# Performance work log

Measured on AMD Instinct MI355X. Metric: run time of the kernel, lower is better.

## Reference

```python
import jax, jax.numpy as jnp
import numpy as np

N_NODES = 100000
N_EDGES = 300000
F = 256


def setup_inputs() -> dict:
    key = jax.random.key(0)
    k1, k2, k3, k4, k5, k6 = jax.random.split(key, 6)
    x = jax.random.normal(k1, (N_NODES, F), dtype=jnp.float32)
    edge_index = jax.random.randint(k2, (2, N_EDGES), 0, N_NODES, dtype=jnp.int32)
    # GCNConv learned params (PyG: lin weight [out,in] applied as x @ W.T; store as [in,out])
    W_conv = jax.random.normal(k3, (F, F), dtype=jnp.float32) / np.sqrt(F)
    b_conv = jax.random.normal(k4, (F,), dtype=jnp.float32) * 0.01
    W_lin = jax.random.normal(k5, (F, 1), dtype=jnp.float32) / np.sqrt(F)
    b_lin = jax.random.normal(k6, (1,), dtype=jnp.float32) * 0.01
    return {"x": x, "edge_index": edge_index, "W_conv": W_conv,
            "b_conv": b_conv, "W_lin": W_lin, "b_lin": b_lin}


def gcn_conv(x, edge_index, W_conv, b_conv):
    N = x.shape[0]
    # add self loops (PyG default add_self_loops=True)
    loop = jnp.arange(N, dtype=edge_index.dtype)
    src = jnp.concatenate([edge_index[0], loop])
    dst = jnp.concatenate([edge_index[1], loop])
    # symmetric normalization: deg over destination, norm = d^-1/2[src]*d^-1/2[dst]
    deg = jax.ops.segment_sum(jnp.ones_like(dst, dtype=x.dtype), dst, num_segments=N)
    dinv = jnp.where(deg > 0, jax.lax.rsqrt(deg), 0.0)
    norm = dinv[src] * dinv[dst]  # [E+N]
    h = x @ W_conv  # [N,F] dense transform first (PyG order)
    msg = h[src] * norm[:, None]  # gather + scale, [E+N, F]
    agg = jax.ops.segment_sum(msg, dst, num_segments=N)  # scatter-add, [N,F]
    return agg + b_conv


def reference(x, edge_index, W_conv, b_conv, W_lin, b_lin):
    h = jax.nn.relu(gcn_conv(x, edge_index, W_conv, b_conv))
    return jax.nn.sigmoid(h @ W_lin + b_lin)  # [N,1]
```

## Files before the change

kernel.cpp:

```cpp
#include <hip/hip_runtime.h>
#include <hip/hip_bf16.h>
#include <math.h>

#define FDIM 256

typedef short bfrag __attribute__((ext_vector_type(8)));
typedef float f32x4 __attribute__((ext_vector_type(4)));

__device__ __forceinline__ short f2bf_rne(float f) {
    uint32_t u = __float_as_uint(f);
    uint32_t r = (u + 0x7FFFu + ((u >> 16) & 1u)) >> 16;
    return (short)r;
}
__device__ __forceinline__ float bf2f(short s) {
    return __uint_as_float(((uint32_t)(uint16_t)s) << 16);
}

#define GLOAD_LDS16(g, l) __builtin_amdgcn_global_load_lds(              \
    (const __attribute__((address_space(1))) void*)(g),                  \
    (__attribute__((address_space(3))) void*)(l), 16, 0, 0)

__global__ void count_kernel(const int* __restrict__ dst, int* __restrict__ counts, int E) {
    int e = blockIdx.x * 256 + threadIdx.x;
    if (e < E) atomicAdd(&counts[dst[e]], 1);
}

__global__ void scan1_kernel(const int* __restrict__ counts, int* __restrict__ blksums, int N) {
    __shared__ int sd[256];
    int tid = threadIdx.x;
    int base = blockIdx.x * 1024 + tid * 4;
    int s = 0;
#pragma unroll
    for (int t = 0; t < 4; ++t) { int i = base + t; if (i < N) s += counts[i]; }
    sd[tid] = s; __syncthreads();
    for (int off = 128; off > 0; off >>= 1) {
        if (tid < off) sd[tid] += sd[tid + off];
        __syncthreads();
    }
    if (tid == 0) blksums[blockIdx.x] = sd[0];
}

__global__ void scan2_kernel(int* __restrict__ blksums, int NB) {
    __shared__ int sd[128];
    int tid = threadIdx.x;
    int v = (tid < NB) ? blksums[tid] : 0;
    sd[tid] = v; __syncthreads();
    for (int off = 1; off < 128; off <<= 1) {
        int t = (tid >= off) ? sd[tid - off] : 0;
        __syncthreads();
        sd[tid] += t;
        __syncthreads();
    }
    if (tid < NB) blksums[tid] = sd[tid] - v;
}

__global__ void scan3_kernel(const int* __restrict__ counts, const int* __restrict__ blksums,
                             int* __restrict__ offsets, int* __restrict__ cursor,
                             float* __restrict__ dinv, int N, int E) {
    __shared__ int sd[256];
    int tid = threadIdx.x;
    int base = blockIdx.x * 1024 + tid * 4;
    int c[4]; int s = 0;
#pragma unroll
    for (int t = 0; t < 4; ++t) { int i = base + t; c[t] = (i < N) ? counts[i] : 0; s += c[t]; }
    sd[tid] = s; __syncthreads();
    int v = s;
    for (int off = 1; off < 256; off <<= 1) {
        int t = (tid >= off) ? sd[tid - off] : 0;
        __syncthreads();
        sd[tid] += t;
        __syncthreads();
    }
    int run = sd[tid] - v + blksums[blockIdx.x];
#pragma unroll
    for (int t = 0; t < 4; ++t) {
        int i = base + t;
        if (i < N) {
            offsets[i] = run;
            cursor[i]  = run;
            dinv[i] = rsqrtf((float)(c[t] + 1));
            run += c[t];
        }
    }
    if (blockIdx.x == 0 && tid == 0) offsets[N] = E;
}

__global__ void fill_kernel(const int* __restrict__ src, const int* __restrict__ dst,
                            int* __restrict__ cursor, const float* __restrict__ dinv,
                            int* __restrict__ csr_src, float* __restrict__ csr_norm, int E) {
    int e = blockIdx.x * 256 + threadIdx.x;
    if (e < E) {
        int s = src[e], d = dst[e];
        int pos = atomicAdd(&cursor[d], 1);
        csr_src[pos]  = s;
        csr_norm[pos] = dinv[s] * dinv[d];
    }
}

__global__ void wsplit_kernel(const float* __restrict__ W,
                              short* __restrict__ Wh, short* __restrict__ Wl) {
    const int k = blockIdx.x;
    const int n = threadIdx.x;
    const float w = W[k * 256 + n];
    const short hi = f2bf_rne(w);
    const short lo = f2bf_rne(w - bf2f(hi));
    const int s = k >> 5, g = (k & 31) >> 3, j = k & 7;
    const size_t idx = (size_t)s * 8192 + g * 2048 + n * 8 + j;
    Wh[idx] = hi; Wl[idx] = lo;
}

__global__ __launch_bounds__(512) void gemm_mfma(const float* __restrict__ X,
                                                 const short* __restrict__ Wth,
                                                 const short* __restrict__ Wtl,
                                                 float* __restrict__ H, int N) {
    __shared__ short Xh[4096], Xl[4096];
    __shared__ short Wh[8192], Wl[8192];

    const int tid  = threadIdx.x;
    const int lane = tid & 63;
    const int wid  = tid >> 6;
    const int wm   = wid >> 2;
    const int wn   = wid & 3;
    const int row0 = blockIdx.x * 128;

    const int sm = tid >> 2, sc = tid & 3;

    f32x4 acc[4][4];
#pragma unroll
    for (int i = 0; i < 4; ++i)
#pragma unroll
        for (int j = 0; j < 4; ++j) acc[i][j] = (f32x4){0.f, 0.f, 0.f, 0.f};

    float4 xv0, xv1;
    {
        const int row = row0 + sm;
        if (row < N) {
            const float* s = X + (size_t)row * FDIM + 8 * sc;
            xv0 = *(const float4*)s; xv1 = *(const float4*)(s + 4);
        } else { xv0 = make_float4(0,0,0,0); xv1 = make_float4(0,0,0,0); }
    }

    const int g   = lane >> 4;
    const int r15 = lane & 15;

    for (int s = 0; s < 8; ++s) {
        {
            const float v[8] = {xv0.x, xv0.y, xv0.z, xv0.w, xv1.x, xv1.y, xv1.z, xv1.w};
            bfrag hi8, lo8;
#pragma unroll
            for (int j = 0; j < 8; ++j) {
                const short h = f2bf_rne(v[j]);
                hi8[j] = h;
                lo8[j] = f2bf_rne(v[j] - bf2f(h));
            }
            *(bfrag*)(&Xh[(sc * 128 + sm) * 8]) = hi8;
            *(bfrag*)(&Xl[(sc * 128 + sm) * 8]) = lo8;
        }
        {
            const short* gh = Wth + s * 8192;
            const short* gl = Wtl + s * 8192;
            const int seg = wid * 512 + lane * 8;
#pragma unroll
            for (int p = 0; p < 2; ++p) {
                GLOAD_LDS16(gh + p * 4096 + seg, &Wh[p * 4096 + wid * 512]);
                GLOAD_LDS16(gl + p * 4096 + seg, &Wl[p * 4096 + wid * 512]);
            }
        }
        __syncthreads();

        if (s < 7) {
            const int row = row0 + sm;
            if (row < N) {
                const float* src = X + (size_t)row * FDIM + (s + 1) * 32 + 8 * sc;
                xv0 = *(const float4*)src; xv1 = *(const float4*)(src + 4);
            } else { xv0 = make_float4(0,0,0,0); xv1 = make_float4(0,0,0,0); }
        }

        bfrag bh[4], bl[4];
#pragma unroll
        for (int ni = 0; ni < 4; ++ni) {
            const int off = (g * 256 + wn * 64 + ni * 16 + r15) * 8;
            bh[ni] = *(const bfrag*)(&Wh[off]);
            bl[ni] = *(const bfrag*)(&Wl[off]);
        }
#pragma unroll
        for (int mi = 0; mi < 4; ++mi) {
            const int off = (g * 128 + wm * 64 + mi * 16 + r15) * 8;
            const bfrag ah = *(const bfrag*)(&Xh[off]);
            const bfrag al = *(const bfrag*)(&Xl[off]);
#pragma unroll
            for (int ni = 0; ni < 4; ++ni) {
                acc[mi][ni] = __builtin_amdgcn_mfma_f32_16x16x32_bf16(ah, bh[ni], acc[mi][ni], 0, 0, 0);
                acc[mi][ni] = __builtin_amdgcn_mfma_f32_16x16x32_bf16(ah, bl[ni], acc[mi][ni], 0, 0, 0);
                acc[mi][ni] = __builtin_amdgcn_mfma_f32_16x16x32_bf16(al, bh[ni], acc[mi][ni], 0, 0, 0);
            }
        }
        __syncthreads();
    }

#pragma unroll
    for (int mi = 0; mi < 4; ++mi) {
        const int rowb = row0 + wm * 64 + mi * 16 + g * 4;
#pragma unroll
        for (int r = 0; r < 4; ++r) {
            const int row = rowb + r;
            if (row < N) {
                float* base = H + (size_t)row * FDIM + wn * 64 + r15;
#pragma unroll
                for (int ni = 0; ni < 4; ++ni) base[ni * 16] = acc[mi][ni][r];
            }
        }
    }
}

__global__ __launch_bounds__(256) void agg_kernel(const float* __restrict__ h,
                                                  const int* __restrict__ offsets,
                                                  const int* __restrict__ csr_src,
                                                  const float* __restrict__ csr_norm,
                                                  const float* __restrict__ dinv,
                                                  const float* __restrict__ b_conv,
                                                  const float* __restrict__ W_lin,
                                                  const float* __restrict__ b_lin,
                                                  float* __restrict__ out, int N) {
    const int wid  = threadIdx.x >> 6;
    const int lane = threadIdx.x & 63;
    const int node = blockIdx.x * 4 + wid;
    if (node >= N) return;

    const float4* __restrict__ h4 = (const float4*)h;
    float4 acc = {0.f, 0.f, 0.f, 0.f};

    const int start = offsets[node];
    const int end   = offsets[node + 1];
    const float di  = dinv[node];

    for (int j = start; j < end; ++j) {
        const int s   = csr_src[j];
        const float w = csr_norm[j];
        const float4 v = h4[(size_t)s * 64 + lane];
        acc.x = fmaf(v.x, w, acc.x);
        acc.y = fmaf(v.y, w, acc.y);
        acc.z = fmaf(v.z, w, acc.z);
        acc.w = fmaf(v.w, w, acc.w);
    }
    {
        const float w = di * di;
        const float4 v = h4[(size_t)node * 64 + lane];
        acc.x = fmaf(v.x, w, acc.x);
        acc.y = fmaf(v.y, w, acc.y);
        acc.z = fmaf(v.z, w, acc.z);
        acc.w = fmaf(v.w, w, acc.w);
    }
    const float4 bc = ((const float4*)b_conv)[lane];
    acc.x = fmaxf(acc.x + bc.x, 0.f);
    acc.y = fmaxf(acc.y + bc.y, 0.f);
    acc.z = fmaxf(acc.z + bc.z, 0.f);
    acc.w = fmaxf(acc.w + bc.w, 0.f);

    const float4 wl = ((const float4*)W_lin)[lane];
    float p = acc.x * wl.x + acc.y * wl.y + acc.z * wl.z + acc.w * wl.w;
#pragma unroll
    for (int off = 32; off > 0; off >>= 1) p += __shfl_xor(p, off);
    if (lane == 0) out[node] = 1.f / (1.f + expf(-(p + b_lin[0])));
}

extern "C" void kernel_launch(void* const* d_in, const int* in_sizes, int n_in,
                              void* d_out, int out_size, void* d_ws, size_t ws_size,
                              hipStream_t stream) {
    const float* x      = (const float*)d_in[0];
    const int*   eidx   = (const int*)d_in[1];
    const float* W_conv = (const float*)d_in[2];
    const float* b_conv = (const float*)d_in[3];
    const float* W_lin  = (const float*)d_in[4];
    const float* b_lin  = (const float*)d_in[5];
    float* out = (float*)d_out;

    const int N = in_sizes[0] / FDIM;
    const int E = in_sizes[1] / 2;
    const int* e_src = eidx;
    const int* e_dst = eidx + E;

    char* p = (char*)d_ws;
    float* h = (float*)p;           p += (size_t)N * FDIM * sizeof(float);
    int* counts   = (int*)p;        p += (size_t)N * sizeof(int);
    int* offsets  = (int*)p;        p += (size_t)(N + 1) * sizeof(int);
    int* cursor   = (int*)p;        p += (size_t)N * sizeof(int);
    float* dinv   = (float*)p;      p += (size_t)N * sizeof(float);
    int* csr_src  = (int*)p;        p += (size_t)E * sizeof(int);
    float* csr_norm = (float*)p;    p += (size_t)E * sizeof(float);
    int* blksums  = (int*)p;        p += 128 * sizeof(int);
    short* Wth    = (short*)p;      p += (size_t)FDIM * FDIM * sizeof(short);
    short* Wtl    = (short*)p;      p += (size_t)FDIM * FDIM * sizeof(short);

    const int NB = (N + 1023) / 1024;

    hipMemsetAsync(counts, 0, (size_t)N * sizeof(int), stream);

    count_kernel<<<(E + 255) / 256, 256, 0, stream>>>(e_dst, counts, E);
    scan1_kernel<<<NB, 256, 0, stream>>>(counts, blksums, N);
    scan2_kernel<<<1, 128, 0, stream>>>(blksums, NB);
    scan3_kernel<<<NB, 256, 0, stream>>>(counts, blksums, offsets, cursor, dinv, N, E);
    fill_kernel<<<(E + 255) / 256, 256, 0, stream>>>(e_src, e_dst, cursor, dinv,
                                                     csr_src, csr_norm, E);

    wsplit_kernel<<<FDIM, FDIM, 0, stream>>>(W_conv, Wth, Wtl);

    gemm_mfma<<<(N + 127) / 128, 512, 0, stream>>>(x, Wth, Wtl, h, N);

    agg_kernel<<<(N + 3) / 4, 256, 0, stream>>>(h, offsets, csr_src, csr_norm, dinv,
                                                b_conv, W_lin, b_lin, out, N);
}
```

Before: 309.3 us.

## Store H as bf16, double-buffer GEMM LDS, change W/X layout, unroll aggregation

The GEMM now writes its output H in bf16 rather than fp32, which halves H's write traffic and the gather traffic in the aggregation kernel. The GEMM also double-buffers its X and W tiles in LDS, prefetching the next stage while the current one computes, and switches to a row-major k-interleaved fragment layout. The aggregation loop is unrolled by two with independent accumulators. Rounding H to bf16 adds error relative to the fp32 reference, and the doubled LDS footprint may reduce occupancy.

Result: faster. 286.8 us (-7.3%).

```diff
diff --git a/kernel.cpp b/kernel.cpp
--- a/kernel.cpp
+++ b/kernel.cpp
@@ -12,8 +12,8 @@
     uint32_t r = (u + 0x7FFFu + ((u >> 16) & 1u)) >> 16;
     return (short)r;
 }
-__device__ __forceinline__ float bf2f(short s) {
-    return __uint_as_float(((uint32_t)(uint16_t)s) << 16);
+__device__ __forceinline__ float bf2f(unsigned short s) {
+    return __uint_as_float(((uint32_t)s) << 16);
 }
 
 #define GLOAD_LDS16(g, l) __builtin_amdgcn_global_load_lds(              \
@@ -103,18 +103,18 @@
     const int n = threadIdx.x;
     const float w = W[k * 256 + n];
     const short hi = f2bf_rne(w);
-    const short lo = f2bf_rne(w - bf2f(hi));
+    const short lo = f2bf_rne(w - bf2f((unsigned short)hi));
     const int s = k >> 5, g = (k & 31) >> 3, j = k & 7;
-    const size_t idx = (size_t)s * 8192 + g * 2048 + n * 8 + j;
+    const size_t idx = (size_t)s * 8192 + n * 32 + g * 8 + j;
     Wh[idx] = hi; Wl[idx] = lo;
 }
 
 __global__ __launch_bounds__(512) void gemm_mfma(const float* __restrict__ X,
                                                  const short* __restrict__ Wth,
                                                  const short* __restrict__ Wtl,
-                                                 float* __restrict__ H, int N) {
-    __shared__ short Xh[4096], Xl[4096];
-    __shared__ short Wh[8192], Wl[8192];
+                                                 unsigned short* __restrict__ Hb, int N) {
+    __shared__ short Xh[2][4096], Xl[2][4096];
+    __shared__ short Wh[2][8192], Wl[2][8192];
 
     const int tid  = threadIdx.x;
     const int lane = tid & 63;
@@ -122,8 +122,9 @@
     const int wm   = wid >> 2;
     const int wn   = wid & 3;
     const int row0 = blockIdx.x * 128;
-
-    const int sm = tid >> 2, sc = tid & 3;
+    const int sm   = tid >> 2;
+    const int g    = lane >> 4;
+    const int r15  = lane & 15;
 
     f32x4 acc[4][4];
 #pragma unroll
@@ -131,63 +132,71 @@
 #pragma unroll
         for (int j = 0; j < 4; ++j) acc[i][j] = (f32x4){0.f, 0.f, 0.f, 0.f};
 
-    float4 xv0, xv1;
+    const int xrow = row0 + sm;
+    const float* xbase = X + (size_t)xrow * FDIM + 8 * (tid & 3);
+
+    float4 xa0, xa1;
+    if (xrow < N) { xa0 = *(const float4*)xbase; xa1 = *(const float4*)(xbase + 4); }
+    else          { xa0 = make_float4(0,0,0,0); xa1 = make_float4(0,0,0,0); }
     {
-        const int row = row0 + sm;
-        if (row < N) {
-            const float* s = X + (size_t)row * FDIM + 8 * sc;
-            xv0 = *(const float4*)s; xv1 = *(const float4*)(s + 4);
-        } else { xv0 = make_float4(0,0,0,0); xv1 = make_float4(0,0,0,0); }
-    }
-
-    const int g   = lane >> 4;
-    const int r15 = lane & 15;
+        const float v[8] = {xa0.x,xa0.y,xa0.z,xa0.w,xa1.x,xa1.y,xa1.z,xa1.w};
+        bfrag hi8, lo8;
+#pragma unroll
+        for (int j = 0; j < 8; ++j) {
+            const short h = f2bf_rne(v[j]);
+            hi8[j] = h; lo8[j] = f2bf_rne(v[j] - bf2f((unsigned short)h));
+        }
+        *(bfrag*)(&Xh[0][tid * 8]) = hi8;
+        *(bfrag*)(&Xl[0][tid * 8]) = lo8;
+    }
+#pragma unroll
+    for (int p = 0; p < 2; ++p) {
+        GLOAD_LDS16(Wth + p * 4096 + wid * 512 + lane * 8, &Wh[0][p * 4096 + wid * 512]);
+        GLOAD_LDS16(Wtl + p * 4096 + wid * 512 + lane * 8, &Wl[0][p * 4096 + wid * 512]);
+    }
+    if (xrow < N) { xa0 = *(const float4*)(xbase + 32); xa1 = *(const float4*)(xbase + 36); }
+    else          { xa0 = make_float4(0,0,0,0); xa1 = make_float4(0,0,0,0); }
+    __syncthreads();
 
     for (int s = 0; s < 8; ++s) {
-        {
-            const float v[8] = {xv0.x, xv0.y, xv0.z, xv0.w, xv1.x, xv1.y, xv1.z, xv1.w};
+        const int cur = s & 1, nxt = cur ^ 1;
+        if (s < 7) {
+            const float v[8] = {xa0.x,xa0.y,xa0.z,xa0.w,xa1.x,xa1.y,xa1.z,xa1.w};
             bfrag hi8, lo8;
 #pragma unroll
             for (int j = 0; j < 8; ++j) {
                 const short h = f2bf_rne(v[j]);
-                hi8[j] = h;
-                lo8[j] = f2bf_rne(v[j] - bf2f(h));
+                hi8[j] = h; lo8[j] = f2bf_rne(v[j] - bf2f((unsigned short)h));
             }
-            *(bfrag*)(&Xh[(sc * 128 + sm) * 8]) = hi8;
-            *(bfrag*)(&Xl[(sc * 128 + sm) * 8]) = lo8;
-        }
-        {
-            const short* gh = Wth + s * 8192;
-            const short* gl = Wtl + s * 8192;
-            const int seg = wid * 512 + lane * 8;
+            *(bfrag*)(&Xh[nxt][tid * 8]) = hi8;
+            *(bfrag*)(&Xl[nxt][tid * 8]) = lo8;
+            const short* gh = Wth + (s + 1) * 8192;
+            const short* gl = Wtl + (s + 1) * 8192;
 #pragma unroll
             for (int p = 0; p < 2; ++p) {
-                GLOAD_LDS16(gh + p * 4096 + seg, &Wh[p * 4096 + wid * 512]);
-                GLOAD_LDS16(gl + p * 4096 + seg, &Wl[p * 4096 + wid * 512]);
+                GLOAD_LDS16(gh + p * 4096 + wid * 512 + lane * 8, &Wh[nxt][p * 4096 + wid * 512]);
+                GLOAD_LDS16(gl + p * 4096 + wid * 512 + lane * 8, &Wl[nxt][p * 4096 + wid * 512]);
             }
         }
-        __syncthreads();
-
-        if (s < 7) {
-            const int row = row0 + sm;
-            if (row < N) {
-                const float* src = X + (size_t)row * FDIM + (s + 1) * 32 + 8 * sc;
-                xv0 = *(const float4*)src; xv1 = *(const float4*)(src + 4);
-            } else { xv0 = make_float4(0,0,0,0); xv1 = make_float4(0,0,0,0); }
+        if (s < 6) {
+            if (xrow < N) {
+                const float* src = xbase + (s + 2) * 32;
+                xa0 = *(const float4*)src; xa1 = *(const float4*)(src + 4);
+            } else { xa0 = make_float4(0,0,0,0); xa1 = make_float4(0,0,0,0); }
         }
 
         bfrag bh[4], bl[4];
 #pragma unroll
         for (int ni = 0; ni < 4; ++ni) {
-            const int off = (g * 256 + wn * 64 + ni * 16 + r15) * 8;
-            bh[ni] = *(const bfrag*)(&Wh[off]);
-            bl[ni] = *(const bfrag*)(&Wl[off]);
+            const int off = ((wn * 64 + ni * 16 + r15) * 4 + g) * 8;
+            bh[ni] = *(const bfrag*)(&Wh[cur][off]);
+            bl[ni] = *(const bfrag*)(&Wl[cur][off]);
         }
 #pragma unroll
         for (int mi = 0; mi < 4; ++mi) {
-            const int off = (g * 128 + wm * 64 + mi * 16 + r15) * 8;
-            const bfrag ah = *(const bfrag*)(&Xh[off]);
-            const bfrag al = *(const bfrag*)(&Xl[off]);
+            const int off = ((wm * 64 + mi * 16 + r15) * 4 + g) * 8;
+            const bfrag ah = *(const bfrag*)(&Xh[cur][off]);
+            const bfrag al = *(const bfrag*)(&Xl[cur][off]);
 #pragma unroll
             for (int ni = 0; ni < 4; ++ni) {
                 acc[mi][ni] = __builtin_amdgcn_mfma_f32_16x16x32_bf16(ah, bh[ni], acc[mi][ni], 0, 0, 0);
@@ -195,7 +204,7 @@
                 acc[mi][ni] = __builtin_amdgcn_mfma_f32_16x16x32_bf16(al, bh[ni], acc[mi][ni], 0, 0, 0);
             }
         }
-        __syncthreads();
+        if (s < 7) __syncthreads();
     }
 
 #pragma unroll
@@ -205,15 +214,16 @@
         for (int r = 0; r < 4; ++r) {
             const int row = rowb + r;
             if (row < N) {
-                float* base = H + (size_t)row * FDIM + wn * 64 + r15;
-#pragma unroll
-                for (int ni = 0; ni < 4; ++ni) base[ni * 16] = acc[mi][ni][r];
+                unsigned short* base = Hb + (size_t)row * FDIM + wn * 64 + r15;
+#pragma unroll
+                for (int ni = 0; ni < 4; ++ni)
+                    base[ni * 16] = (unsigned short)f2bf_rne(acc[mi][ni][r]);
             }
         }
     }
 }
 
-__global__ __launch_bounds__(256) void agg_kernel(const float* __restrict__ h,
+__global__ __launch_bounds__(256) void agg_kernel(const unsigned short* __restrict__ hb,
                                                   const int* __restrict__ offsets,
                                                   const int* __restrict__ csr_src,
                                                   const float* __restrict__ csr_norm,
@@ -227,38 +237,45 @@
     const int node = blockIdx.x * 4 + wid;
     if (node >= N) return;
 
-    const float4* __restrict__ h4 = (const float4*)h;
-    float4 acc = {0.f, 0.f, 0.f, 0.f};
+    float a0 = 0.f, a1 = 0.f, a2 = 0.f, a3 = 0.f;
+    float c0 = 0.f, c1 = 0.f, c2 = 0.f, c3 = 0.f;
 
     const int start = offsets[node];
     const int end   = offsets[node + 1];
     const float di  = dinv[node];
 
-    for (int j = start; j < end; ++j) {
-        const int s   = csr_src[j];
-        const float w = csr_norm[j];
-        const float4 v = h4[(size_t)s * 64 + lane];
-        acc.x = fmaf(v.x, w, acc.x);
-        acc.y = fmaf(v.y, w, acc.y);
-        acc.z = fmaf(v.z, w, acc.z);
-        acc.w = fmaf(v.w, w, acc.w);
+    int j = start;
+    for (; j + 1 < end; j += 2) {
+        const int   s0 = csr_src[j],     s1 = csr_src[j + 1];
+        const float w0 = csr_norm[j],    w1 = csr_norm[j + 1];
+        const ushort4 v0 = *((const ushort4*)(hb + (size_t)s0 * FDIM) + lane);
+        const ushort4 v1 = *((const ushort4*)(hb + (size_t)s1 * FDIM) + lane);
+        a0 = fmaf(bf2f(v0.x), w0, a0); a1 = fmaf(bf2f(v0.y), w0, a1);
+        a2 = fmaf(bf2f(v0.z), w0, a2); a3 = fmaf(bf2f(v0.w), w0, a3);
+        c0 = fmaf(bf2f(v1.x), w1, c0); c1 = fmaf(bf2f(v1.y), w1, c1);
+        c2 = fmaf(bf2f(v1.z), w1, c2); c3 = fmaf(bf2f(v1.w), w1, c3);
+    }
+    if (j < end) {
+        const int   s0 = csr_src[j];
+        const float w0 = csr_norm[j];
+        const ushort4 v0 = *((const ushort4*)(hb + (size_t)s0 * FDIM) + lane);
+        a0 = fmaf(bf2f(v0.x), w0, a0); a1 = fmaf(bf2f(v0.y), w0, a1);
+        a2 = fmaf(bf2f(v0.z), w0, a2); a3 = fmaf(bf2f(v0.w), w0, a3);
     }
     {
         const float w = di * di;
-        const float4 v = h4[(size_t)node * 64 + lane];
-        acc.x = fmaf(v.x, w, acc.x);
-        acc.y = fmaf(v.y, w, acc.y);
-        acc.z = fmaf(v.z, w, acc.z);
-        acc.w = fmaf(v.w, w, acc.w);
-    }
+        const ushort4 v = *((const ushort4*)(hb + (size_t)node * FDIM) + lane);
+        a0 = fmaf(bf2f(v.x), w, a0); a1 = fmaf(bf2f(v.y), w, a1);
+        a2 = fmaf(bf2f(v.z), w, a2); a3 = fmaf(bf2f(v.w), w, a3);
+    }
+    a0 += c0; a1 += c1; a2 += c2; a3 += c3;
+
     const float4 bc = ((const float4*)b_conv)[lane];
-    acc.x = fmaxf(acc.x + bc.x, 0.f);
-    acc.y = fmaxf(acc.y + bc.y, 0.f);
-    acc.z = fmaxf(acc.z + bc.z, 0.f);
-    acc.w = fmaxf(acc.w + bc.w, 0.f);
+    a0 = fmaxf(a0 + bc.x, 0.f); a1 = fmaxf(a1 + bc.y, 0.f);
+    a2 = fmaxf(a2 + bc.z, 0.f); a3 = fmaxf(a3 + bc.w, 0.f);
 
     const float4 wl = ((const float4*)W_lin)[lane];
-    float p = acc.x * wl.x + acc.y * wl.y + acc.z * wl.z + acc.w * wl.w;
+    float p = a0 * wl.x + a1 * wl.y + a2 * wl.z + a3 * wl.w;
 #pragma unroll
     for (int off = 32; off > 0; off >>= 1) p += __shfl_xor(p, off);
     if (lane == 0) out[node] = 1.f / (1.f + expf(-(p + b_lin[0])));
@@ -281,7 +298,7 @@
     const int* e_dst = eidx + E;
 
     char* p = (char*)d_ws;
-    float* h = (float*)p;           p += (size_t)N * FDIM * sizeof(float);
+    unsigned short* hb = (unsigned short*)p; p += (size_t)N * FDIM * sizeof(unsigned short);
     int* counts   = (int*)p;        p += (size_t)N * sizeof(int);
     int* offsets  = (int*)p;        p += (size_t)(N + 1) * sizeof(int);
     int* cursor   = (int*)p;        p += (size_t)N * sizeof(int);
@@ -305,8 +322,8 @@
 
     wsplit_kernel<<<FDIM, FDIM, 0, stream>>>(W_conv, Wth, Wtl);
 
-    gemm_mfma<<<(N + 127) / 128, 512, 0, stream>>>(x, Wth, Wtl, h, N);
-
-    agg_kernel<<<(N + 3) / 4, 256, 0, stream>>>(h, offsets, csr_src, csr_norm, dinv,
+    gemm_mfma<<<(N + 127) / 128, 512, 0, stream>>>(x, Wth, Wtl, hb, N);
+
+    agg_kernel<<<(N + 3) / 4, 256, 0, stream>>>(hb, offsets, csr_src, csr_norm, dinv,
                                                 b_conv, W_lin, b_lin, out, N);
 }
```
